# Performance work log

Hardware: AMD Instinct MI355X
Metric: run time of the kernel (lower is better)

## Reference

```python
import jax, jax.numpy as jnp
import numpy as np

U, V, A = 100000, 50000, 5000   # n_users, n_videos, n_vloggers
D = 64                           # latent_dim_rec
N_LAYERS = 3                     # VAGNN_n_layers
NNZ_UI, NNZ_UA, NNZ_G2, NNZ_G4 = 4_000_000, 2_000_000, 200_000, 2_000_000
BATCH = 1024

def spmm(rows, cols, vals, x, n_rows):
    # sparse.mm(COO(rows, cols, vals), x) -> [n_rows, d]
    return jax.ops.segment_sum(vals[:, None] * x[cols], rows, num_segments=n_rows)

def one_propagate(rows, cols, vals, a_feat, b_feat):
    # LightGCN propagation: mean over layer-0..n embeddings (running sum, no stack)
    n = a_feat.shape[0] + b_feat.shape[0]
    feats = jnp.concatenate([a_feat, b_feat], axis=0)
    acc, cur = feats, feats
    for _ in range(N_LAYERS):
        cur = spmm(rows, cols, vals, cur, n)
        acc = acc + cur
    light = acc / (N_LAYERS + 1)
    return light[:a_feat.shape[0]], light[a_feat.shape[0]:]

def l2norm(x):
    # F.normalize(x, dim=1), eps=1e-12
    return x / jnp.maximum(jnp.linalg.norm(x, axis=1, keepdims=True), 1e-12)

def setup_inputs() -> dict:
    key = jax.random.key(0)
    ks = jax.random.split(key, 16)
    return {
        'emb_user':    jax.random.normal(ks[0], (U, D), jnp.float32) * 0.1,
        'emb_video':   jax.random.normal(ks[1], (V, D), jnp.float32) * 0.1,
        'emb_vlogger': jax.random.normal(ks[2], (A, D), jnp.float32) * 0.1,
        'q':           jax.random.normal(ks[3], (D, D), jnp.float32) * 0.1,
        'ui_rows': jax.random.randint(ks[4], (NNZ_UI,), 0, U + V, jnp.int32),
        'ui_cols': jax.random.randint(ks[5], (NNZ_UI,), 0, U + V, jnp.int32),
        'ui_vals': jax.random.uniform(ks[6], (NNZ_UI,), jnp.float32) * 0.01,
        'ua_rows': jax.random.randint(ks[7], (NNZ_UA,), 0, U + A, jnp.int32),
        'ua_cols': jax.random.randint(ks[8], (NNZ_UA,), 0, U + A, jnp.int32),
        'ua_vals': jax.random.uniform(ks[9], (NNZ_UA,), jnp.float32) * 0.01,
        'g2_rows': jax.random.randint(ks[10], (NNZ_G2,), 0, A, jnp.int32),
        'g2_cols': jax.random.randint(ks[11], (NNZ_G2,), 0, V, jnp.int32),
        'g2_vals': jax.random.uniform(ks[12], (NNZ_G2,), jnp.float32) * 0.01,
        'g4_rows': jax.random.randint(ks[13], (NNZ_G4,), 0, V, jnp.int32),
        'g4_cols': jax.random.randint(ks[14], (NNZ_G4,), 0, U, jnp.int32),
        'g4_vals': jax.random.uniform(ks[15], (NNZ_G4,), jnp.float32) * 0.01,
        'vlogger_list': jax.random.randint(jax.random.fold_in(key, 100), (V,), 0, A, jnp.int32),
        'users': jax.random.randint(jax.random.fold_in(key, 101), (BATCH,), 0, U, jnp.int32),
    }

def reference(emb_user, emb_video, emb_vlogger, q,
              ui_rows, ui_cols, ui_vals,
              ua_rows, ua_cols, ua_vals,
              g2_rows, g2_cols, g2_vals,
              g4_rows, g4_cols, g4_vals,
              vlogger_list, users):
    # computer()
    atom_u, atom_v = one_propagate(ui_rows, ui_cols, ui_vals, emb_user, emb_video)
    atom_a = l2norm(spmm(g2_rows, g2_cols, g2_vals, atom_v, A))
    non_u, non_a = one_propagate(ua_rows, ua_cols, ua_vals, emb_user, emb_vlogger)
    non_v = l2norm(spmm(g4_rows, g4_cols, g4_vals, non_u, V))
    # getUsersRating()
    u_a, u_n = atom_u[users], non_u[users]                 # [B, D]
    vl_a, vl_n = atom_a[vlogger_list], non_a[vlogger_list]  # [V, D]
    ui = jax.nn.sigmoid(u_a @ atom_v.T + u_n @ non_v.T)      # [B, V]
    ua = jax.nn.sigmoid(u_a @ vl_a.T + u_n @ vl_n.T)         # [B, V]
    vid = (atom_v + non_v) * 0.5
    vlog = (vl_a + vl_n) * 0.5
    w = jax.nn.sigmoid(jnp.sum((vid @ q) * vlog, axis=1))    # [V]
    return w * ui + (1.0 - w) * ua
```

## Files before the change

kernel.cpp:

```cpp
#include <hip/hip_runtime.h>
#include <hip/hip_bf16.h>

#define U_N 100000
#define V_N 50000
#define A_N 5000

typedef float4 f4;
typedef unsigned int u32;
typedef __attribute__((ext_vector_type(8))) short bf16x8;
typedef __attribute__((ext_vector_type(4))) float f32x4;

__device__ inline float bflo(u32 p) { return __uint_as_float(p << 16); }
__device__ inline float bfhi(u32 p) { return __uint_as_float(p & 0xffff0000u); }
__device__ inline u32 f2bf(float f) {
  u32 u = __float_as_uint(f);
  return (u + 0x7fffu + ((u >> 16) & 1u)) >> 16;
}
__device__ inline u32 pack2(float lo, float hi) {
  return f2bf(lo) | (f2bf(hi) << 16);
}
__device__ inline bf16x8 ld8(const u32* p) {
  uint4 u = *(const uint4*)p;
  return __builtin_bit_cast(bf16x8, u);
}

__global__ void k_concat2b(const float* __restrict__ a, int na,
                           const float* __restrict__ b, int nb,
                           u32* __restrict__ curH, float* __restrict__ acc) {
  int total4 = (na + nb) * 16;
  for (int i = blockIdx.x * blockDim.x + threadIdx.x; i < total4;
       i += gridDim.x * blockDim.x) {
    int fi = i * 4;
    f4 v = (fi < na * 64) ? *(const f4*)(a + fi)
                          : *(const f4*)(b + (fi - na * 64));
    *(f4*)(acc + fi) = v;
    uint2 h; h.x = pack2(v.x, v.y); h.y = pack2(v.z, v.w);
    *(uint2*)(curH + (fi >> 1)) = h;
  }
}

__global__ void k_count(const int* __restrict__ rows, int nnz, int* __restrict__ cnt) {
  for (int i = blockIdx.x * blockDim.x + threadIdx.x; i < nnz;
       i += gridDim.x * blockDim.x)
    atomicAdd(&cnt[rows[i]], 1);
}

__global__ void k_bsum(const int* __restrict__ cnt, int n, int* __restrict__ bsum) {
  __shared__ int red[1024];
  int t = threadIdx.x;
  int i = blockIdx.x * 1024 + t;
  red[t] = (i < n) ? cnt[i] : 0;
  __syncthreads();
  for (int off = 512; off; off >>= 1) {
    if (t < off) red[t] += red[t + off];
    __syncthreads();
  }
  if (t == 0) bsum[blockIdx.x] = red[0];
}

__global__ void k_bscan(int* __restrict__ bsum, int nb) {
  if (threadIdx.x == 0) {
    int run = 0;
    for (int i = 0; i < nb; ++i) {
      int c = bsum[i];
      bsum[i] = run;
      run += c;
    }
  }
}

__global__ void k_bapply(const int* __restrict__ cnt, int n,
                         const int* __restrict__ bsum,
                         int* __restrict__ rp, int* __restrict__ pos) {
  __shared__ int sc[1024];
  int t = threadIdx.x;
  int i = blockIdx.x * 1024 + t;
  int c = (i < n) ? cnt[i] : 0;
  sc[t] = c;
  __syncthreads();
  #pragma unroll
  for (int off = 1; off < 1024; off <<= 1) {
    int v = (t >= off) ? sc[t - off] : 0;
    __syncthreads();
    sc[t] += v;
    __syncthreads();
  }
  int val = bsum[blockIdx.x] + sc[t] - c;
  if (i < n) {
    rp[i] = val;
    pos[i] = val;
    if (i == n - 1) rp[n] = val + c;
  }
}

__global__ void k_fillw(const int* __restrict__ rows, const int* __restrict__ cols,
                        const float* __restrict__ vals, int nnz,
                        int* __restrict__ pos, int2* __restrict__ ep,
                        int nrows, int win) {
  int tid = blockIdx.x * blockDim.x + threadIdx.x;
  int stride = gridDim.x * blockDim.x;
  for (int r0 = 0; r0 < nrows; r0 += win) {
    int r1 = min(r0 + win, nrows);
    for (int i = tid; i < nnz; i += stride) {
      int r = rows[i];
      if (r >= r0 && r < r1) {
        int slot = atomicAdd(&pos[r], 1);
        ep[slot] = make_int2(cols[i], __float_as_int(vals[i]));
      }
    }
  }
}

__global__ void k_fill(const int* __restrict__ rows, const int* __restrict__ cols,
                       const float* __restrict__ vals, int nnz,
                       int* __restrict__ pos, int2* __restrict__ ep) {
  for (int i = blockIdx.x * blockDim.x + threadIdx.x; i < nnz;
       i += gridDim.x * blockDim.x) {
    int slot = atomicAdd(&pos[rows[i]], 1);
    ep[slot] = make_int2(cols[i], __float_as_int(vals[i]));
  }
}

__global__ void k_mark(const int* __restrict__ users, int nb,
                       int* __restrict__ flag, int* __restrict__ rcount,
                       int* __restrict__ rlist) {
  int b = blockIdx.x * blockDim.x + threadIdx.x;
  if (b < nb) {
    int u = users[b];
    if (atomicExch(&flag[u], 1) == 0) {
      int m = atomicAdd(rcount, 1);
      rlist[m] = u;
    }
  }
}

__device__ __forceinline__ void spmm_row(
    int row, const int* __restrict__ rp, const int2* __restrict__ ep,
    const u32* __restrict__ inH, int instrU,
    u32* __restrict__ outH, int ostrU, int ocolU,
    float* __restrict__ acc, int l2n, int wout, int lane, int eg, int du) {
  int e0 = rp[row], e1 = rp[row + 1];
  float s[8] = {0.f, 0.f, 0.f, 0.f, 0.f, 0.f, 0.f, 0.f};
  int e = e0 + eg;
  for (; e + 8 < e1; e += 16) {
    int2 ed0 = ep[e];
    int2 ed1 = ep[e + 8];
    float v0 = __int_as_float(ed0.y), v1 = __int_as_float(ed1.y);
    uint4 x0 = *(const uint4*)(inH + (size_t)ed0.x * instrU + du);
    uint4 x1 = *(const uint4*)(inH + (size_t)ed1.x * instrU + du);
    s[0] = fmaf(v0, bflo(x0.x), s[0]); s[1] = fmaf(v0, bfhi(x0.x), s[1]);
    s[2] = fmaf(v0, bflo(x0.y), s[2]); s[3] = fmaf(v0, bfhi(x0.y), s[3]);
    s[4] = fmaf(v0, bflo(x0.z), s[4]); s[5] = fmaf(v0, bfhi(x0.z), s[5]);
    s[6] = fmaf(v0, bflo(x0.w), s[6]); s[7] = fmaf(v0, bfhi(x0.w), s[7]);
    s[0] = fmaf(v1, bflo(x1.x), s[0]); s[1] = fmaf(v1, bfhi(x1.x), s[1]);
    s[2] = fmaf(v1, bflo(x1.y), s[2]); s[3] = fmaf(v1, bfhi(x1.y), s[3]);
    s[4] = fmaf(v1, bflo(x1.z), s[4]); s[5] = fmaf(v1, bfhi(x1.z), s[5]);
    s[6] = fmaf(v1, bflo(x1.w), s[6]); s[7] = fmaf(v1, bfhi(x1.w), s[7]);
  }
  if (e < e1) {
    int2 ed0 = ep[e];
    float v0 = __int_as_float(ed0.y);
    uint4 x0 = *(const uint4*)(inH + (size_t)ed0.x * instrU + du);
    s[0] = fmaf(v0, bflo(x0.x), s[0]); s[1] = fmaf(v0, bfhi(x0.x), s[1]);
    s[2] = fmaf(v0, bflo(x0.y), s[2]); s[3] = fmaf(v0, bfhi(x0.y), s[3]);
    s[4] = fmaf(v0, bflo(x0.z), s[4]); s[5] = fmaf(v0, bfhi(x0.z), s[5]);
    s[6] = fmaf(v0, bflo(x0.w), s[6]); s[7] = fmaf(v0, bfhi(x0.w), s[7]);
  }
  #pragma unroll
  for (int j = 0; j < 8; ++j) {
    s[j] += __shfl_xor(s[j], 8);
    s[j] += __shfl_xor(s[j], 16);
    s[j] += __shfl_xor(s[j], 32);
  }
  if (l2n) {
    float ss = 0.f;
    #pragma unroll
    for (int j = 0; j < 8; ++j) ss = fmaf(s[j], s[j], ss);
    ss += __shfl_xor(ss, 1);
    ss += __shfl_xor(ss, 2);
    ss += __shfl_xor(ss, 4);
    float inv = 1.0f / fmaxf(sqrtf(ss), 1e-12f);
    #pragma unroll
    for (int j = 0; j < 8; ++j) s[j] *= inv;
  }
  if (eg == 0) {
    if (wout) {
      uint4 o;
      o.x = pack2(s[0], s[1]); o.y = pack2(s[2], s[3]);
      o.z = pack2(s[4], s[5]); o.w = pack2(s[6], s[7]);
      *(uint4*)(outH + (size_t)row * ostrU + ocolU + du) = o;
    }
    if (acc) {
      float* ap = acc + (size_t)row * 64 + (lane & 7) * 8;
      f4 a0 = *(f4*)ap, a1 = *(f4*)(ap + 4);
      a0.x += s[0]; a0.y += s[1]; a0.z += s[2]; a0.w += s[3];
      a1.x += s[4]; a1.y += s[5]; a1.z += s[6]; a1.w += s[7];
      *(f4*)ap = a0; *(f4*)(ap + 4) = a1;
    }
  }
}

__global__ void k_spmm_b(const int* __restrict__ rp, const int2* __restrict__ ep,
                         int nrows, int rbase,
                         const u32* __restrict__ inH, int instrU,
                         u32* __restrict__ outH, int ostrU, int ocolU,
                         float* __restrict__ acc, int l2n, int wout) {
  int lane = threadIdx.x & 63;
  int w = (blockIdx.x * blockDim.x + threadIdx.x) >> 6;
  int nw = (gridDim.x * blockDim.x) >> 6;
  int eg = lane >> 3;
  int du = (lane & 7) * 4;
  for (int r = w; r < nrows; r += nw)
    spmm_row(rbase + r, rp, ep, inH, instrU, outH, ostrU, ocolU, acc, l2n, wout,
             lane, eg, du);
}

__global__ void k_spmm_b_list(const int* __restrict__ rp, const int2* __restrict__ ep,
                              const int* __restrict__ rlist, const int* __restrict__ rcount,
                              const u32* __restrict__ inH, int instrU,
                              float* __restrict__ acc) {
  int lane = threadIdx.x & 63;
  int w = (blockIdx.x * blockDim.x + threadIdx.x) >> 6;
  int nw = (gridDim.x * blockDim.x) >> 6;
  int eg = lane >> 3;
  int du = (lane & 7) * 4;
  int m = *rcount;
  for (int r = w; r < m; r += nw)
    spmm_row(rlist[r], rp, ep, inH, instrU, nullptr, 0, 0, acc, 0, 0,
             lane, eg, du);
}

__global__ void k_scale_ua(float* __restrict__ acc, u32* __restrict__ UAuH) {
  int total4 = (U_N + A_N) * 16;
  for (int i = blockIdx.x * blockDim.x + threadIdx.x; i < total4;
       i += gridDim.x * blockDim.x) {
    int fi = i * 4;
    f4 v = *(f4*)(acc + fi);
    v.x *= 0.25f; v.y *= 0.25f; v.z *= 0.25f; v.w *= 0.25f;
    *(f4*)(acc + fi) = v;
    if (fi < U_N * 64) {
      uint2 h; h.x = pack2(v.x, v.y); h.y = pack2(v.z, v.w);
      *(uint2*)(UAuH + (fi >> 1)) = h;
    }
  }
}

__global__ void k_scale_ui(float* __restrict__ acc, u32* __restrict__ VAH) {
  int total4 = (U_N + V_N) * 16;
  for (int i = blockIdx.x * blockDim.x + threadIdx.x; i < total4;
       i += gridDim.x * blockDim.x) {
    int fi = i * 4;
    f4 v = *(f4*)(acc + fi);
    v.x *= 0.25f; v.y *= 0.25f; v.z *= 0.25f; v.w *= 0.25f;
    *(f4*)(acc + fi) = v;
    if (fi >= U_N * 64) {
      int rem = fi - U_N * 64;
      int row = rem >> 6, col = rem & 63;
      uint2 h; h.x = pack2(v.x, v.y); h.y = pack2(v.z, v.w);
      *(uint2*)(VAH + (size_t)row * 64 + (col >> 1)) = h;
    }
  }
}

__global__ void k_gather_u(const int* __restrict__ users,
                           const float* __restrict__ accUI,
                           const float* __restrict__ accUA,
                           u32* __restrict__ UcatH) {
  int b = blockIdx.x;
  int t = threadIdx.x;
  int u = users[b];
  UcatH[b * 64 + t] = pack2(accUI[(size_t)u * 64 + 2 * t], accUI[(size_t)u * 64 + 2 * t + 1]);
  UcatH[b * 64 + 32 + t] = pack2(accUA[(size_t)u * 64 + 2 * t], accUA[(size_t)u * 64 + 2 * t + 1]);
}

__global__ void k_gather_vb(const int* __restrict__ vlist,
                            const u32* __restrict__ atomAH,
                            const float* __restrict__ accUA,
                            u32* __restrict__ VBH) {
  int v = blockIdx.x * 4 + (threadIdx.x >> 5);
  int t = threadIdx.x & 31;
  int a = vlist[v];
  VBH[(size_t)v * 64 + t] = atomAH[(size_t)a * 32 + t];
  VBH[(size_t)v * 64 + 32 + t] =
      pack2(accUA[(size_t)(U_N + a) * 64 + 2 * t], accUA[(size_t)(U_N + a) * 64 + 2 * t + 1]);
}

__global__ void k_w(const u32* __restrict__ VAH, const u32* __restrict__ VBH,
                    const float* __restrict__ q, float* __restrict__ wv) {
  __shared__ float qs[64 * 64];
  for (int i = threadIdx.x; i < 4096; i += blockDim.x) qs[i] = q[i];
  __syncthreads();
  int lane = threadIdx.x & 63;
  int v = blockIdx.x * 4 + (threadIdx.x >> 6);
  if (v >= V_N) return;
  int half = lane & 1;
  u32 pa0 = VAH[(size_t)v * 64 + (lane >> 1)];
  u32 pa1 = VAH[(size_t)v * 64 + 32 + (lane >> 1)];
  u32 pb0 = VBH[(size_t)v * 64 + (lane >> 1)];
  u32 pb1 = VBH[(size_t)v * 64 + 32 + (lane >> 1)];
  float vid = 0.5f * ((half ? bfhi(pa0) : bflo(pa0)) + (half ? bfhi(pa1) : bflo(pa1)));
  float vlog = 0.5f * ((half ? bfhi(pb0) : bflo(pb0)) + (half ? bfhi(pb1) : bflo(pb1)));
  float s = 0.0f;
  for (int d = 0; d < 64; ++d)
    s = fmaf(__shfl(vid, d, 64), qs[d * 64 + lane], s);
  float t = s * vlog;
  #pragma unroll
  for (int off = 32; off; off >>= 1) t += __shfl_xor(t, off, 64);
  if (lane == 0) wv[v] = 1.0f / (1.0f + __expf(-t));
}

#define SPAD 68
__global__ __launch_bounds__(256) void k_rating_mfma(
    const u32* __restrict__ UcatH, const u32* __restrict__ VAH,
    const u32* __restrict__ VBH, const float* __restrict__ wv,
    float* __restrict__ out) {
  __shared__ u32 sVA[64 * SPAD];
  __shared__ u32 sVB[64 * SPAD];
  int t = threadIdx.x;
  int n0 = blockIdx.x * 64;
  for (int i = t; i < 1024; i += 256) {
    int row = i >> 4, c4 = (i & 15) * 4;
    int v = n0 + row;
    uint4 a = make_uint4(0, 0, 0, 0), b = make_uint4(0, 0, 0, 0);
    if (v < V_N) {
      a = *(const uint4*)(VAH + (size_t)v * 64 + c4);
      b = *(const uint4*)(VBH + (size_t)v * 64 + c4);
    }
    *(uint4*)(&sVA[row * SPAD + c4]) = a;
    *(uint4*)(&sVB[row * SPAD + c4]) = b;
  }
  __syncthreads();
  int lane = t & 63, wave = t >> 6;
  int m0 = (blockIdx.y * 4 + wave) * 32;
  int rr = lane & 15, g = lane >> 4;
  f32x4 accA[2][4], accB[2][4];
  #pragma unroll
  for (int i = 0; i < 2; ++i)
    #pragma unroll
    for (int j = 0; j < 4; ++j) {
      accA[i][j] = (f32x4){0.f, 0.f, 0.f, 0.f};
      accB[i][j] = (f32x4){0.f, 0.f, 0.f, 0.f};
    }
  const u32* uc0 = UcatH + (size_t)(m0 + rr) * 64 + g * 4;
  #pragma unroll
  for (int ks = 0; ks < 4; ++ks) {
    bf16x8 a0 = ld8(uc0 + ks * 16);
    bf16x8 a1 = ld8(uc0 + 16 * 64 + ks * 16);
    #pragma unroll
    for (int j = 0; j < 4; ++j) {
      int so = (j * 16 + rr) * SPAD + ks * 16 + g * 4;
      bf16x8 bA = __builtin_bit_cast(bf16x8, *(const uint4*)(&sVA[so]));
      bf16x8 bB = __builtin_bit_cast(bf16x8, *(const uint4*)(&sVB[so]));
      accA[0][j] = __builtin_amdgcn_mfma_f32_16x16x32_bf16(a0, bA, accA[0][j], 0, 0, 0);
      accA[1][j] = __builtin_amdgcn_mfma_f32_16x16x32_bf16(a1, bA, accA[1][j], 0, 0, 0);
      accB[0][j] = __builtin_amdgcn_mfma_f32_16x16x32_bf16(a0, bB, accB[0][j], 0, 0, 0);
      accB[1][j] = __builtin_amdgcn_mfma_f32_16x16x32_bf16(a1, bB, accB[1][j], 0, 0, 0);
    }
  }
  #pragma unroll
  for (int j = 0; j < 4; ++j) {
    int v = n0 + j * 16 + rr;
    if (v >= V_N) continue;
    float wvv = wv[v];
    #pragma unroll
    for (int i = 0; i < 2; ++i) {
      #pragma unroll
      for (int reg = 0; reg < 4; ++reg) {
        int u = m0 + i * 16 + g * 4 + reg;
        float sa = 1.0f / (1.0f + __expf(-accA[i][j][reg]));
        float sb = 1.0f / (1.0f + __expf(-accB[i][j][reg]));
        __builtin_nontemporal_store(wvv * sa + (1.0f - wvv) * sb,
                                    &out[(size_t)u * V_N + v]);
      }
    }
  }
}

extern "C" void kernel_launch(void* const* d_in, const int* in_sizes, int n_in,
                              void* d_out, int out_size, void* d_ws, size_t ws_size,
                              hipStream_t stream) {
  const float* emb_user    = (const float*)d_in[0];
  const float* emb_video   = (const float*)d_in[1];
  const float* emb_vlogger = (const float*)d_in[2];
  const float* q           = (const float*)d_in[3];
  const int*   ui_rows = (const int*)d_in[4];
  const int*   ui_cols = (const int*)d_in[5];
  const float* ui_vals = (const float*)d_in[6];
  const int*   ua_rows = (const int*)d_in[7];
  const int*   ua_cols = (const int*)d_in[8];
  const float* ua_vals = (const float*)d_in[9];
  const int*   g2_rows = (const int*)d_in[10];
  const int*   g2_cols = (const int*)d_in[11];
  const float* g2_vals = (const float*)d_in[12];
  const int*   g4_rows = (const int*)d_in[13];
  const int*   g4_cols = (const int*)d_in[14];
  const float* g4_vals = (const float*)d_in[15];
  const int*   vlist   = (const int*)d_in[16];
  const int*   users   = (const int*)d_in[17];
  int nnz_ui = in_sizes[4], nnz_ua = in_sizes[7];
  int nnz_g2 = in_sizes[10], nnz_g4 = in_sizes[13];

  float* ws = (float*)d_ws;
  float* accUI = ws;
  float* accUA = ws + 9600000;
  u32*   curH  = (u32*)(ws + 16320000);
  u32*   nxtH  = (u32*)(ws + 21120000);
  u32*   VAH   = (u32*)(ws + 25920000);
  u32*   VBH   = (u32*)(ws + 29120000);
  u32*   UAuH  = (u32*)(ws + 32320000);
  u32*   UcatH = (u32*)(ws + 35520000);
  u32*   atomAH= (u32*)(ws + 35585536);
  float* wv    = ws + 35745536;
  int*   bsum  = (int*)(ws + 35795536);
  int*   ib    = (int*)(ws + 35800000);
  int*   flag   = (int*)VBH;
  int*   rcount = flag + 100000;
  int*   rlist  = flag + 100016;

  const int nUI = U_N + V_N, nUA = U_N + A_N;
  auto nr_pad = [](int nrows) { return (size_t)((nrows + 1 + 15) & ~15); };

  auto build_csr = [&](const int* rows, const int* cols, const float* vals,
                       int nnz, int nrows, int win, int* rp, int* pos, int2* ep) {
    hipMemsetAsync(pos, 0, (size_t)nrows * 4, stream);
    k_count<<<2048, 256, 0, stream>>>(rows, nnz, pos);
    int nb = (nrows + 1023) / 1024;
    k_bsum<<<nb, 1024, 0, stream>>>(pos, nrows, bsum);
    k_bscan<<<1, 64, 0, stream>>>(bsum, nb);
    k_bapply<<<nb, 1024, 0, stream>>>(pos, nrows, bsum, rp, pos);
    if (nrows <= win)
      k_fill<<<2048, 256, 0, stream>>>(rows, cols, vals, nnz, pos, ep);
    else
      k_fillw<<<2048, 256, 0, stream>>>(rows, cols, vals, nnz, pos, ep, nrows, win);
  };

  {
    size_t NR = nr_pad(nUI);
    int* rp = ib; int* pos = ib + NR; int2* ep = (int2*)(ib + 2 * NR);
    build_csr(ui_rows, ui_cols, ui_vals, nnz_ui, nUI, 16384, rp, pos, ep);
    k_concat2b<<<2048, 256, 0, stream>>>(emb_user, U_N, emb_video, V_N, curH, accUI);
    hipMemsetAsync(flag, 0, (size_t)(100016) * 4, stream);
    k_mark<<<4, 256, 0, stream>>>(users, 1024, flag, rcount, rlist);
    k_spmm_b<<<2048, 256, 0, stream>>>(rp, ep, nUI, 0, curH, 32, nxtH, 32, 0, accUI, 0, 1);
    k_spmm_b<<<2048, 256, 0, stream>>>(rp, ep, nUI, 0, nxtH, 32, curH, 32, 0, accUI, 0, 1);
    k_spmm_b<<<2048, 256, 0, stream>>>(rp, ep, V_N, U_N, curH, 32, nullptr, 0, 0, accUI, 0, 0);
    k_spmm_b_list<<<256, 256, 0, stream>>>(rp, ep, rlist, rcount, curH, 32, accUI);
  }
  {
    size_t NR = nr_pad(nUA);
    int* rp = ib; int* pos = ib + NR; int2* ep = (int2*)(ib + 2 * NR);
    build_csr(ua_rows, ua_cols, ua_vals, nnz_ua, nUA, 16384, rp, pos, ep);
    k_concat2b<<<2048, 256, 0, stream>>>(emb_user, U_N, emb_vlogger, A_N, curH, accUA);
    k_spmm_b<<<2048, 256, 0, stream>>>(rp, ep, nUA, 0, curH, 32, nxtH, 32, 0, accUA, 0, 1);
    k_spmm_b<<<2048, 256, 0, stream>>>(rp, ep, nUA, 0, nxtH, 32, curH, 32, 0, accUA, 0, 1);
    k_spmm_b<<<2048, 256, 0, stream>>>(rp, ep, nUA, 0, curH, 32, nullptr, 0, 0, accUA, 0, 0);
  }
  k_scale_ua<<<2048, 256, 0, stream>>>(accUA, UAuH);
  k_scale_ui<<<2048, 256, 0, stream>>>(accUI, VAH);
  size_t NR4 = nr_pad(V_N), NR2 = nr_pad(A_N);
  int* rp4 = ib; int* pos4 = ib + NR4; int2* ep4 = (int2*)(ib + 2 * NR4);
  int* ib2 = (int*)(ep4 + nnz_g4);
  int* rp2 = ib2; int* pos2 = ib2 + NR2; int2* ep2 = (int2*)(ib2 + 2 * NR2);
  build_csr(g4_rows, g4_cols, g4_vals, nnz_g4, V_N, 8192, rp4, pos4, ep4);
  build_csr(g2_rows, g2_cols, g2_vals, nnz_g2, A_N, 8192, rp2, pos2, ep2);
  k_spmm_b<<<2048, 256, 0, stream>>>(rp2, ep2, A_N, 0, VAH, 64, atomAH, 32, 0, nullptr, 1, 1);
  k_spmm_b<<<2048, 256, 0, stream>>>(rp4, ep4, V_N, 0, UAuH, 32, VAH, 64, 32, nullptr, 1, 1);
  k_gather_u<<<1024, 32, 0, stream>>>(users, accUI, accUA, UcatH);
  k_gather_vb<<<12500, 128, 0, stream>>>(vlist, atomAH, accUA, VBH);
  k_w<<<12500, 256, 0, stream>>>(VAH, VBH, q, wv);
  dim3 gridR((V_N + 63) / 64, 1024 / 128);
  k_rating_mfma<<<gridR, 256, 0, stream>>>(UcatH, VAH, VBH, wv, (float*)d_out);
}
```

Baseline: 1.428 ms.

## Schedule windowed CSR fill via per-XCD work queues and vectorize count loads

Replaces the windowed CSR fill, which swept every row window in turn across all threads, with a dynamic work queue of (window, edge-chunk) items. Items are split into eight queues by window index modulo 8, and each block starts on the queue matching its XCC id. The aim is to keep each window's pos and ep atomics local to one XCD's L2 and to let blocks work on different windows at the same time instead of in lockstep. The count kernel also reads rows four at a time as int4. The costs are an extra memset, atomic queue traffic with block barriers per item, and reliance on reading the XCC hardware register.

Result: slower. 1.977 ms (+38.5%).

```diff
diff --git a/kernel.cpp b/kernel.cpp
--- a/kernel.cpp
+++ b/kernel.cpp
@@ -4,6 +4,7 @@
 #define U_N 100000
 #define V_N 50000
 #define A_N 5000
+#define FCS 16384
 
 typedef float4 f4;
 typedef unsigned int u32;
@@ -22,6 +23,12 @@
 __device__ inline bf16x8 ld8(const u32* p) {
   uint4 u = *(const uint4*)p;
   return __builtin_bit_cast(bf16x8, u);
+}
+
+__device__ __forceinline__ u32 xcc_id() {
+  u32 x;
+  asm volatile("s_getreg_b32 %0, hwreg(HW_REG_XCC_ID)" : "=s"(x));
+  return x & 7;
 }
 
 __global__ void k_concat2b(const float* __restrict__ a, int na,
@@ -40,8 +47,17 @@
 }
 
 __global__ void k_count(const int* __restrict__ rows, int nnz, int* __restrict__ cnt) {
-  for (int i = blockIdx.x * blockDim.x + threadIdx.x; i < nnz;
-       i += gridDim.x * blockDim.x)
+  int nq = nnz >> 2;
+  int tid = blockIdx.x * blockDim.x + threadIdx.x;
+  int stride = gridDim.x * blockDim.x;
+  for (int q = tid; q < nq; q += stride) {
+    int4 r4 = *(const int4*)(rows + q * 4);
+    atomicAdd(&cnt[r4.x], 1);
+    atomicAdd(&cnt[r4.y], 1);
+    atomicAdd(&cnt[r4.z], 1);
+    atomicAdd(&cnt[r4.w], 1);
+  }
+  for (int i = nq * 4 + tid; i < nnz; i += stride)
     atomicAdd(&cnt[rows[i]], 1);
 }
 
@@ -93,19 +109,36 @@
   }
 }
 
-__global__ void k_fillw(const int* __restrict__ rows, const int* __restrict__ cols,
+__global__ void k_fillq(const int* __restrict__ rows, const int* __restrict__ cols,
                         const float* __restrict__ vals, int nnz,
                         int* __restrict__ pos, int2* __restrict__ ep,
-                        int nrows, int win) {
-  int tid = blockIdx.x * blockDim.x + threadIdx.x;
-  int stride = gridDim.x * blockDim.x;
-  for (int r0 = 0; r0 < nrows; r0 += win) {
-    int r1 = min(r0 + win, nrows);
-    for (int i = tid; i < nnz; i += stride) {
-      int r = rows[i];
-      if (r >= r0 && r < r1) {
-        int slot = atomicAdd(&pos[r], 1);
-        ep[slot] = make_int2(cols[i], __float_as_int(vals[i]));
+                        int nrows, int win, int* __restrict__ xq) {
+  int nw = (nrows + win - 1) / win;
+  int nchunk = (nnz + FCS - 1) / FCS;
+  u32 xcd = xcc_id();
+  __shared__ int sitem;
+  for (int pass = 0; pass < 8; ++pass) {
+    int q = ((int)xcd + pass) & 7;
+    int nwq = (nw > q) ? ((nw - 1 - q) >> 3) + 1 : 0;
+    int items = nwq * nchunk;
+    if (items == 0) continue;
+    for (;;) {
+      __syncthreads();
+      if (threadIdx.x == 0) sitem = atomicAdd(&xq[q], 1);
+      __syncthreads();
+      int item = sitem;
+      if (item >= items) break;
+      int wi = item / nchunk;
+      int chunk = item - wi * nchunk;
+      int w = q + (wi << 3);
+      int r0 = w * win, r1 = min(r0 + win, nrows);
+      int e0 = chunk * FCS, e1 = min(e0 + FCS, nnz);
+      for (int i = e0 + threadIdx.x; i < e1; i += blockDim.x) {
+        int r = rows[i];
+        if (r >= r0 && r < r1) {
+          int slot = atomicAdd(&pos[r], 1);
+          ep[slot] = make_int2(cols[i], __float_as_int(vals[i]));
+        }
       }
     }
   }
@@ -412,6 +445,7 @@
   u32*   atomAH= (u32*)(ws + 35585536);
   float* wv    = ws + 35745536;
   int*   bsum  = (int*)(ws + 35795536);
+  int*   xq    = (int*)(ws + 35795808);
   int*   ib    = (int*)(ws + 35800000);
   int*   flag   = (int*)VBH;
   int*   rcount = flag + 100000;
@@ -428,10 +462,13 @@
     k_bsum<<<nb, 1024, 0, stream>>>(pos, nrows, bsum);
     k_bscan<<<1, 64, 0, stream>>>(bsum, nb);
     k_bapply<<<nb, 1024, 0, stream>>>(pos, nrows, bsum, rp, pos);
-    if (nrows <= win)
+    if (nrows <= win) {
       k_fill<<<2048, 256, 0, stream>>>(rows, cols, vals, nnz, pos, ep);
-    else
-      k_fillw<<<2048, 256, 0, stream>>>(rows, cols, vals, nnz, pos, ep, nrows, win);
+    } else {
+      hipMemsetAsync(xq, 0, 32, stream);
+      k_fillq<<<2048, 256, 0, stream>>>(rows, cols, vals, nnz, pos, ep,
+                                        nrows, win, xq);
+    }
   };
 
   {
```
